# Kernel tuning notes

Hardware: AMD Instinct MI355X
Metric: run time of the kernel (lower is better)

Reference implementation:

```python
import jax, jax.numpy as jnp
from jax import lax
import numpy as np

B, L, N = 128, 16, 20000
H_IN, H, H_T = 512, 1024, 128


def setup_inputs() -> dict:
    key = jax.random.key(0)
    ks = jax.random.split(key, 8)
    def xav(k, shape):
        fan_in, fan_out = shape[1], shape[0]
        a = jnp.sqrt(6.0 / (fan_in + fan_out))
        return jax.random.uniform(k, shape, jnp.float32, -a, a)
    v = jax.random.uniform(ks[0], (B, L, N), jnp.float32)
    t = jax.random.uniform(ks[1], (B, L), jnp.float32)
    W_down = xav(ks[2], (H_IN, N))
    Wt_up_w = xav(ks[3], (H_T, 1))
    Wt_up_b = jnp.zeros((H_T,), jnp.float32)
    W_vt = xav(ks[4], (H_IN, H_IN + H_T))
    k_lstm = 1.0 / jnp.sqrt(H)
    W_ih = jax.random.uniform(ks[5], (4 * H, H_IN), jnp.float32, -k_lstm, k_lstm)
    W_hh = jax.random.uniform(ks[6], (4 * H, H), jnp.float32, -k_lstm, k_lstm)
    b_ih = jnp.zeros((4 * H,), jnp.float32)
    b_hh = jnp.zeros((4 * H,), jnp.float32)
    lin_w = xav(ks[7], (1, H))
    lin_b = jnp.zeros((1,), jnp.float32)
    return {"v": v, "t": t, "W_down": W_down, "Wt_up_w": Wt_up_w,
            "Wt_up_b": Wt_up_b, "W_vt": W_vt, "W_ih": W_ih, "W_hh": W_hh,
            "b_ih": b_ih, "b_hh": b_hh, "lin_w": lin_w, "lin_b": lin_b}


def reference(v, t, W_down, Wt_up_w, Wt_up_b, W_vt, W_ih, W_hh, b_ih, b_hh, lin_w, lin_b):
    b, rw_len, n = v.shape
    h_dim = W_hh.shape[1]
    # W_down: [B,L,N] @ [N,H_in] -> [B,L,H_in]
    vd = jnp.einsum('bln,dn->bld', v, W_down)
    # Wt_up: scalar time -> [B,L,H_t]
    te = t[..., None] * Wt_up_w[:, 0] + Wt_up_b
    vt = jnp.concatenate([vd, te], axis=-1)          # [B,L,H_in+H_t]
    inputs = jnp.einsum('blk,ik->bli', vt, W_vt)     # [B,L,H_in]
    # precompute input-side LSTM gate projections for all steps
    xg = jnp.einsum('bli,gi->blg', inputs, W_ih) + b_ih  # [B,L,4H]
    xg = jnp.swapaxes(xg, 0, 1)                      # [L,B,4H] for scan

    def step(carry, xg_t):
        h, c = carry
        gates = xg_t + h @ W_hh.T + b_hh             # [B,4H]
        i, f, g, o = jnp.split(gates, 4, axis=-1)    # PyTorch gate order i,f,g,o
        i = jax.nn.sigmoid(i)
        f = jax.nn.sigmoid(f)
        g = jnp.tanh(g)
        o = jax.nn.sigmoid(o)
        c = f * c + i * g
        h = o * jnp.tanh(c)
        return (h, c), None

    h0 = jnp.zeros((b, h_dim), v.dtype)
    c0 = jnp.zeros((b, h_dim), v.dtype)
    (h, _), _ = lax.scan(step, (h0, c0), xg)
    pred = h @ lin_w.T + lin_b                       # [B,1]
    return pred
```

## Files before the change

### kernel.cpp

```cpp
#include <hip/hip_runtime.h>

typedef _Float16 f16;
typedef _Float16 f16x2 __attribute__((ext_vector_type(2)));
typedef _Float16 f16x4 __attribute__((ext_vector_type(4)));
typedef _Float16 f16x8 __attribute__((ext_vector_type(8)));
typedef float f32x4 __attribute__((ext_vector_type(4)));

__device__ __forceinline__ f32x4 mfma16(f16x8 a, f16x8 b, f32x4 c) {
  return __builtin_amdgcn_mfma_f32_16x16x32_f16(a, b, c, 0, 0, 0);
}

__device__ __forceinline__ float sigmoid_(float x) { return 1.f / (1.f + __expf(-x)); }
__device__ __forceinline__ float tanh_(float x) { return 1.f - 2.f / (__expf(2.f * x) + 1.f); }

__global__ void cvt_kernel(const float* __restrict__ src, f16* __restrict__ dst, int n4) {
  int i = blockIdx.x * 256 + threadIdx.x;
  if (i < n4) {
    float4 v = ((const float4*)src)[i];
    f16x4 h = {(f16)v.x, (f16)v.y, (f16)v.z, (f16)v.w};
    ((f16x4*)dst)[i] = h;
  }
}

__global__ __launch_bounds__(256, 2) void gemm1_kernel(
    const float* __restrict__ A, const f16* __restrict__ B, f16* __restrict__ P) {
  constexpr int K = 20000;
  __shared__ f16 Al[128][40];
  __shared__ f16 Bl[128][40];
  int tid = threadIdx.x;
  int split = blockIdx.x;
  int m0 = (blockIdx.y >> 2) * 128, n0 = (blockIdx.y & 3) * 128;
  int it0 = (split * 625) >> 3, it1 = ((split + 1) * 625) >> 3;
  int wid = tid >> 6, lane = tid & 63;
  int wm = wid & 1, wn = wid >> 1;
  int lm = lane & 15, quad = lane >> 4;
  int srow = tid >> 1, sseg = (tid & 1) * 16;

  const float* aptr = A + (size_t)(m0 + srow) * K + sseg;
  const f16* bptr = B + (size_t)(n0 + srow) * K + sseg;

  float4 Ar0, Ar1, Ar2, Ar3;
  f16x8 Br0, Br1;
  {
    int k0 = it0 * 32;
    Ar0 = *(const float4*)(aptr + k0);
    Ar1 = *(const float4*)(aptr + k0 + 4);
    Ar2 = *(const float4*)(aptr + k0 + 8);
    Ar3 = *(const float4*)(aptr + k0 + 12);
    Br0 = *(const f16x8*)(bptr + k0);
    Br1 = *(const f16x8*)(bptr + k0 + 8);
  }

  f32x4 acc[4][4];
#pragma unroll
  for (int i = 0; i < 4; ++i)
#pragma unroll
    for (int j = 0; j < 4; ++j) acc[i][j] = (f32x4){0.f, 0.f, 0.f, 0.f};

  for (int it = it0; it < it1; ++it) {
    __syncthreads();
    f16x8 pa0 = {(f16)Ar0.x, (f16)Ar0.y, (f16)Ar0.z, (f16)Ar0.w,
                 (f16)Ar1.x, (f16)Ar1.y, (f16)Ar1.z, (f16)Ar1.w};
    f16x8 pa1 = {(f16)Ar2.x, (f16)Ar2.y, (f16)Ar2.z, (f16)Ar2.w,
                 (f16)Ar3.x, (f16)Ar3.y, (f16)Ar3.z, (f16)Ar3.w};
    *(f16x8*)&Al[srow][sseg] = pa0;
    *(f16x8*)&Al[srow][sseg + 8] = pa1;
    *(f16x8*)&Bl[srow][sseg] = Br0;
    *(f16x8*)&Bl[srow][sseg + 8] = Br1;
    if (it + 1 < it1) {
      int kn = (it + 1) * 32;
      Ar0 = *(const float4*)(aptr + kn);
      Ar1 = *(const float4*)(aptr + kn + 4);
      Ar2 = *(const float4*)(aptr + kn + 8);
      Ar3 = *(const float4*)(aptr + kn + 12);
      Br0 = *(const f16x8*)(bptr + kn);
      Br1 = *(const f16x8*)(bptr + kn + 8);
    }
    __syncthreads();
    f16x8 af[4], bf[4];
#pragma unroll
    for (int mi = 0; mi < 4; ++mi) af[mi] = *(const f16x8*)&Al[wm * 64 + mi * 16 + lm][quad * 8];
#pragma unroll
    for (int ni = 0; ni < 4; ++ni) bf[ni] = *(const f16x8*)&Bl[wn * 64 + ni * 16 + lm][quad * 8];
#pragma unroll
    for (int mi = 0; mi < 4; ++mi)
#pragma unroll
      for (int ni = 0; ni < 4; ++ni) acc[mi][ni] = mfma16(af[mi], bf[ni], acc[mi][ni]);
  }
  size_t base = (size_t)split * 2048;
#pragma unroll
  for (int mi = 0; mi < 4; ++mi)
#pragma unroll
    for (int ni = 0; ni < 4; ++ni)
#pragma unroll
      for (int r = 0; r < 4; ++r) {
        int row = m0 + wm * 64 + mi * 16 + quad * 4 + r;
        int col = n0 + wn * 64 + ni * 16 + lm;
        P[(base + row) * 512 + col] = (f16)acc[mi][ni][r];
      }
}

__global__ void build_vt_kernel(const f16* __restrict__ P, const float* __restrict__ t,
                                const float* __restrict__ wtw, const float* __restrict__ wtb,
                                f16* __restrict__ vt) {
  int m = blockIdx.x;
  float tv = t[m];
  for (int c = threadIdx.x; c < 640; c += 256) {
    float val;
    if (c < 512) {
      val = 0.f;
#pragma unroll
      for (int s = 0; s < 8; ++s) val += (float)P[((size_t)s * 2048 + m) * 512 + c];
    } else {
      val = tv * wtw[c - 512] + wtb[c - 512];
    }
    vt[(size_t)m * 640 + c] = (f16)val;
  }
}

template <int EPI>
__global__ __launch_bounds__(256, 2) void gemm128_kernel(
    const f16* __restrict__ A, const f16* __restrict__ B, f16* __restrict__ out,
    const float* __restrict__ bias0, const float* __restrict__ bias1, int K_iters, int N) {
  __shared__ f16 Al[128][40];
  __shared__ f16 Bl[128][40];
  int tid = threadIdx.x;
  int m0 = blockIdx.y * 128, n0 = blockIdx.x * 128;
  int wid = tid >> 6, lane = tid & 63;
  int wm = wid & 1, wn = wid >> 1;
  int lm = lane & 15, quad = lane >> 4;
  int K = K_iters * 32;

  f32x4 acc[4][4];
#pragma unroll
  for (int i = 0; i < 4; ++i)
#pragma unroll
    for (int j = 0; j < 4; ++j) acc[i][j] = (f32x4){0.f, 0.f, 0.f, 0.f};

  for (int it = 0; it < K_iters; ++it) {
    int k0 = it * 32;
    __syncthreads();
#pragma unroll
    for (int i = 0; i < 2; ++i) {
      int slot = tid + i * 256;
      int row = slot >> 2, seg = slot & 3;
      *(f16x8*)&Al[row][seg * 8] = *(const f16x8*)(A + (size_t)(m0 + row) * K + k0 + seg * 8);
      *(f16x8*)&Bl[row][seg * 8] = *(const f16x8*)(B + (size_t)(n0 + row) * K + k0 + seg * 8);
    }
    __syncthreads();
    f16x8 af[4], bf[4];
#pragma unroll
    for (int mi = 0; mi < 4; ++mi) af[mi] = *(const f16x8*)&Al[wm * 64 + mi * 16 + lm][quad * 8];
#pragma unroll
    for (int ni = 0; ni < 4; ++ni) bf[ni] = *(const f16x8*)&Bl[wn * 64 + ni * 16 + lm][quad * 8];
#pragma unroll
    for (int mi = 0; mi < 4; ++mi)
#pragma unroll
      for (int ni = 0; ni < 4; ++ni) acc[mi][ni] = mfma16(af[mi], bf[ni], acc[mi][ni]);
  }
#pragma unroll
  for (int mi = 0; mi < 4; ++mi)
#pragma unroll
    for (int ni = 0; ni < 4; ++ni)
#pragma unroll
      for (int r = 0; r < 4; ++r) {
        int row = m0 + wm * 64 + mi * 16 + quad * 4 + r;
        int col = n0 + wn * 64 + ni * 16 + lm;
        float val = acc[mi][ni][r];
        if (EPI == 0) {
          out[(size_t)row * N + col] = (f16)val;
        } else {
          int l = row & 15, b = row >> 4;
          out[(size_t)(l * 128 + b) * N + col] = (f16)(val + bias0[col] + bias1[col]);
        }
      }
}

__global__ __launch_bounds__(256, 1) void lstm_step2_kernel(
    const f16* __restrict__ h_in, const f16* __restrict__ Whh,
    const f16* __restrict__ xg_l, float* __restrict__ cT, f16* __restrict__ h_out) {
  __shared__ f16 Alf[32 * 1032];
  __shared__ float gl[4][32][17];
  __shared__ f16 hx[32][18];
  int tid = threadIdx.x;
  int w = tid >> 6, lane = tid & 63;
  int lm = lane & 15, quad = lane >> 4;
  int h0 = blockIdx.x * 16;
  int b0 = blockIdx.y * 32;

#pragma unroll
  for (int i = 0; i < 16; ++i) {
    int idx = i * 256 + tid;
    int r = idx >> 7, c8 = (idx & 127) * 8;
    *(f16x8*)&Alf[r * 1032 + c8] = *(const f16x8*)(h_in + (size_t)(b0 + r) * 1024 + c8);
  }
  const f16* wrow = Whh + ((size_t)(w << 10) + h0 + lm) * 1024 + quad * 8;
  f16x8 Bv[8];
#pragma unroll
  for (int j = 0; j < 8; ++j) Bv[j] = *(const f16x8*)(wrow + j * 32);
  f32x4 acc0 = {0.f, 0.f, 0.f, 0.f}, acc1 = {0.f, 0.f, 0.f, 0.f};
  __syncthreads();
#pragma unroll
  for (int it = 0; it < 32; ++it) {
    f16x8 bfr = Bv[it & 7];
    if (it < 24) Bv[it & 7] = *(const f16x8*)(wrow + (it + 8) * 32);
    f16x8 a0 = *(const f16x8*)&Alf[lm * 1032 + it * 32 + quad * 8];
    f16x8 a1 = *(const f16x8*)&Alf[(16 + lm) * 1032 + it * 32 + quad * 8];
    acc0 = mfma16(a0, bfr, acc0);
    acc1 = mfma16(a1, bfr, acc1);
  }
#pragma unroll
  for (int r = 0; r < 4; ++r) {
    gl[w][quad * 4 + r][lm] = acc0[r];
    gl[w][16 + quad * 4 + r][lm] = acc1[r];
  }
  __syncthreads();
#pragma unroll
  for (int half = 0; half < 2; ++half) {
    int b = tid & 31, hl = (tid >> 5) + half * 8;
    int gb = b0 + b, gh = h0 + hl;
    const f16* xr = xg_l + (size_t)gb * 4096 + gh;
    float gi = (float)xr[0] + gl[0][b][hl];
    float gf = (float)xr[1024] + gl[1][b][hl];
    float gg = (float)xr[2048] + gl[2][b][hl];
    float go = (float)xr[3072] + gl[3][b][hl];
    float iv = sigmoid_(gi), fv = sigmoid_(gf), gv = tanh_(gg), ov = sigmoid_(go);
    size_t ci = (size_t)gh * 128 + gb;
    float cc = fv * cT[ci] + iv * gv;
    cT[ci] = cc;
    hx[b][hl] = (f16)(ov * tanh_(cc));
  }
  __syncthreads();
  {
    int b = tid >> 3, e = (tid & 7) * 2;
    f16x2 hv = {hx[b][e], hx[b][e + 1]};
    *(f16x2*)(h_out + (size_t)(b0 + b) * 1024 + h0 + e) = hv;
  }
}

__global__ void pred_kernel(const f16* __restrict__ h, const float* __restrict__ w,
                            const float* __restrict__ b, float* __restrict__ out) {
  int bb = blockIdx.x, tid = threadIdx.x;
  f16x4 hv = *(const f16x4*)(h + (size_t)bb * 1024 + tid * 4);
  float4 wv = *(const float4*)(w + tid * 4);
  float s = (float)hv[0] * wv.x + (float)hv[1] * wv.y + (float)hv[2] * wv.z + (float)hv[3] * wv.w;
#pragma unroll
  for (int off = 32; off > 0; off >>= 1) s += __shfl_down(s, off);
  __shared__ float red[4];
  if ((tid & 63) == 0) red[tid >> 6] = s;
  __syncthreads();
  if (tid == 0) out[bb] = red[0] + red[1] + red[2] + red[3] + b[0];
}

extern "C" void kernel_launch(void* const* d_in, const int* in_sizes, int n_in,
                              void* d_out, int out_size, void* d_ws, size_t ws_size,
                              hipStream_t stream) {
  (void)in_sizes; (void)n_in; (void)out_size; (void)ws_size;
  const float* v      = (const float*)d_in[0];
  const float* t      = (const float*)d_in[1];
  const float* W_down = (const float*)d_in[2];
  const float* Wt_w   = (const float*)d_in[3];
  const float* Wt_b   = (const float*)d_in[4];
  const float* W_vt   = (const float*)d_in[5];
  const float* W_ih   = (const float*)d_in[6];
  const float* W_hh   = (const float*)d_in[7];
  const float* b_ih   = (const float*)d_in[8];
  const float* b_hh   = (const float*)d_in[9];
  const float* lin_w  = (const float*)d_in[10];
  const float* lin_b  = (const float*)d_in[11];

  char* ws = (char*)d_ws;
  constexpr size_t OFF_WDOWN = 0;
  constexpr size_t OFF_WVT   = 20480000;
  constexpr size_t OFF_WIH   = 21135360;
  constexpr size_t OFF_WHH   = 25329664;
  constexpr size_t OFF_VT    = 33718272;
  constexpr size_t OFF_IN    = 36339712;
  constexpr size_t OFF_XG    = 38436864;
  constexpr size_t OFF_H0    = 55214080;
  constexpr size_t OFF_C     = 55476224;
  constexpr size_t OFF_H1    = 56000512;

  f16* wdown16 = (f16*)(ws + OFF_WDOWN);
  f16* wvt16   = (f16*)(ws + OFF_WVT);
  f16* wih16   = (f16*)(ws + OFF_WIH);
  f16* whh16   = (f16*)(ws + OFF_WHH);
  f16* vt16    = (f16*)(ws + OFF_VT);
  f16* in16    = (f16*)(ws + OFF_IN);
  f16* pxg     = (f16*)(ws + OFF_XG);
  float* cT    = (float*)(ws + OFF_C);
  f16* hb[2]   = {(f16*)(ws + OFF_H0), (f16*)(ws + OFF_H1)};

  hipMemsetAsync(ws + OFF_H0, 0, 786432, stream);

  cvt_kernel<<<10000, 256, 0, stream>>>(W_down, wdown16, 2560000);
  cvt_kernel<<<320, 256, 0, stream>>>(W_vt, wvt16, 81920);
  cvt_kernel<<<2048, 256, 0, stream>>>(W_ih, wih16, 524288);
  cvt_kernel<<<4096, 256, 0, stream>>>(W_hh, whh16, 1048576);

  gemm1_kernel<<<dim3(8, 64), 256, 0, stream>>>(v, wdown16, pxg);
  build_vt_kernel<<<2048, 256, 0, stream>>>(pxg, t, Wt_w, Wt_b, vt16);
  gemm128_kernel<0><<<dim3(4, 16), 256, 0, stream>>>(vt16, wvt16, in16, nullptr, nullptr, 20, 512);
  gemm128_kernel<1><<<dim3(32, 16), 256, 0, stream>>>(in16, wih16, pxg, b_ih, b_hh, 16, 4096);

  for (int s = 0; s < 16; ++s) {
    lstm_step2_kernel<<<dim3(64, 4), 256, 0, stream>>>(
        hb[s & 1], whh16, pxg + (size_t)s * 128 * 4096, cT, hb[(s + 1) & 1]);
  }
  pred_kernel<<<128, 256, 0, stream>>>(hb[0], lin_w, lin_b, (float*)d_out);
}
```

Before: 544.5 us.

## Fuse W_down conversion into GEMM, merge weight casts, retile small GEMMs

The separate fp32->fp16 pass over W_down is dropped. gemm1 now loads fp32 W_down directly and converts it in registers, which removes a full write and re-read of a 20 MB weight. The split-K factor for gemm1 goes from 8 to 16 with higher occupancy, and build_vt sums 16 partials. The remaining three weight casts are merged into one launch, and the two follow-up GEMMs use smaller templated tiles so more blocks run. The tradeoff is twice the partial-sum traffic and more conversion work inside the main GEMM loop.

```diff
diff --git a/kernel.cpp b/kernel.cpp
--- a/kernel.cpp
+++ b/kernel.cpp
@@ -13,42 +13,52 @@
 __device__ __forceinline__ float sigmoid_(float x) { return 1.f / (1.f + __expf(-x)); }
 __device__ __forceinline__ float tanh_(float x) { return 1.f - 2.f / (__expf(2.f * x) + 1.f); }
 
-__global__ void cvt_kernel(const float* __restrict__ src, f16* __restrict__ dst, int n4) {
+__global__ void cvt3_kernel(const float* __restrict__ s0, f16* __restrict__ d0, int n0,
+                            const float* __restrict__ s1, f16* __restrict__ d1, int n1,
+                            const float* __restrict__ s2, f16* __restrict__ d2, int n2) {
   int i = blockIdx.x * 256 + threadIdx.x;
-  if (i < n4) {
-    float4 v = ((const float4*)src)[i];
-    f16x4 h = {(f16)v.x, (f16)v.y, (f16)v.z, (f16)v.w};
-    ((f16x4*)dst)[i] = h;
-  }
-}
-
-__global__ __launch_bounds__(256, 2) void gemm1_kernel(
-    const float* __restrict__ A, const f16* __restrict__ B, f16* __restrict__ P) {
+  const float* s;
+  f16* d;
+  int j;
+  if (i < n0) {
+    s = s0; d = d0; j = i;
+  } else if (i < n0 + n1) {
+    s = s1; d = d1; j = i - n0;
+  } else if (i < n0 + n1 + n2) {
+    s = s2; d = d2; j = i - n0 - n1;
+  } else {
+    return;
+  }
+  float4 v = ((const float4*)s)[j];
+  f16x4 h = {(f16)v.x, (f16)v.y, (f16)v.z, (f16)v.w};
+  ((f16x4*)d)[j] = h;
+}
+
+__global__ __launch_bounds__(256, 3) void gemm1_kernel(
+    const float* __restrict__ A, const float* __restrict__ B, f16* __restrict__ P) {
   constexpr int K = 20000;
-  __shared__ f16 Al[128][40];
-  __shared__ f16 Bl[128][40];
+  __shared__ f16 Al[128][44];
+  __shared__ f16 Bl[128][44];
   int tid = threadIdx.x;
   int split = blockIdx.x;
   int m0 = (blockIdx.y >> 2) * 128, n0 = (blockIdx.y & 3) * 128;
-  int it0 = (split * 625) >> 3, it1 = ((split + 1) * 625) >> 3;
+  int it0 = (split * 625) >> 4, it1 = ((split + 1) * 625) >> 4;
   int wid = tid >> 6, lane = tid & 63;
   int wm = wid & 1, wn = wid >> 1;
   int lm = lane & 15, quad = lane >> 4;
   int srow = tid >> 1, sseg = (tid & 1) * 16;
 
   const float* aptr = A + (size_t)(m0 + srow) * K + sseg;
-  const f16* bptr = B + (size_t)(n0 + srow) * K + sseg;
-
-  float4 Ar0, Ar1, Ar2, Ar3;
-  f16x8 Br0, Br1;
+  const float* bptr = B + (size_t)(n0 + srow) * K + sseg;
+
+  float4 Ar[4], Br[4];
   {
     int k0 = it0 * 32;
-    Ar0 = *(const float4*)(aptr + k0);
-    Ar1 = *(const float4*)(aptr + k0 + 4);
-    Ar2 = *(const float4*)(aptr + k0 + 8);
-    Ar3 = *(const float4*)(aptr + k0 + 12);
-    Br0 = *(const f16x8*)(bptr + k0);
-    Br1 = *(const f16x8*)(bptr + k0 + 8);
+#pragma unroll
+    for (int j = 0; j < 4; ++j) {
+      Ar[j] = *(const float4*)(aptr + k0 + j * 4);
+      Br[j] = *(const float4*)(bptr + k0 + j * 4);
+    }
   }
 
   f32x4 acc[4][4];
@@ -59,33 +69,38 @@
 
   for (int it = it0; it < it1; ++it) {
     __syncthreads();
-    f16x8 pa0 = {(f16)Ar0.x, (f16)Ar0.y, (f16)Ar0.z, (f16)Ar0.w,
-                 (f16)Ar1.x, (f16)Ar1.y, (f16)Ar1.z, (f16)Ar1.w};
-    f16x8 pa1 = {(f16)Ar2.x, (f16)Ar2.y, (f16)Ar2.z, (f16)Ar2.w,
-                 (f16)Ar3.x, (f16)Ar3.y, (f16)Ar3.z, (f16)Ar3.w};
-    *(f16x8*)&Al[srow][sseg] = pa0;
-    *(f16x8*)&Al[srow][sseg + 8] = pa1;
-    *(f16x8*)&Bl[srow][sseg] = Br0;
-    *(f16x8*)&Bl[srow][sseg + 8] = Br1;
+    {
+      f16x8 pa0 = {(f16)Ar[0].x, (f16)Ar[0].y, (f16)Ar[0].z, (f16)Ar[0].w,
+                   (f16)Ar[1].x, (f16)Ar[1].y, (f16)Ar[1].z, (f16)Ar[1].w};
+      f16x8 pa1 = {(f16)Ar[2].x, (f16)Ar[2].y, (f16)Ar[2].z, (f16)Ar[2].w,
+                   (f16)Ar[3].x, (f16)Ar[3].y, (f16)Ar[3].z, (f16)Ar[3].w};
+      f16x8 pb0 = {(f16)Br[0].x, (f16)Br[0].y, (f16)Br[0].z, (f16)Br[0].w,
+                   (f16)Br[1].x, (f16)Br[1].y, (f16)Br[1].z, (f16)Br[1].w};
+      f16x8 pb1 = {(f16)Br[2].x, (f16)Br[2].y, (f16)Br[2].z, (f16)Br[2].w,
+                   (f16)Br[3].x, (f16)Br[3].y, (f16)Br[3].z, (f16)Br[3].w};
+      *(f16x8*)&Al[srow][sseg] = pa0;
+      *(f16x8*)&Al[srow][sseg + 8] = pa1;
+      *(f16x8*)&Bl[srow][sseg] = pb0;
+      *(f16x8*)&Bl[srow][sseg + 8] = pb1;
+    }
     if (it + 1 < it1) {
       int kn = (it + 1) * 32;
-      Ar0 = *(const float4*)(aptr + kn);
-      Ar1 = *(const float4*)(aptr + kn + 4);
-      Ar2 = *(const float4*)(aptr + kn + 8);
-      Ar3 = *(const float4*)(aptr + kn + 12);
-      Br0 = *(const f16x8*)(bptr + kn);
-      Br1 = *(const f16x8*)(bptr + kn + 8);
+#pragma unroll
+      for (int j = 0; j < 4; ++j) {
+        Ar[j] = *(const float4*)(aptr + kn + j * 4);
+        Br[j] = *(const float4*)(bptr + kn + j * 4);
+      }
     }
     __syncthreads();
-    f16x8 af[4], bf[4];
+    f16x8 af[4];
 #pragma unroll
     for (int mi = 0; mi < 4; ++mi) af[mi] = *(const f16x8*)&Al[wm * 64 + mi * 16 + lm][quad * 8];
 #pragma unroll
-    for (int ni = 0; ni < 4; ++ni) bf[ni] = *(const f16x8*)&Bl[wn * 64 + ni * 16 + lm][quad * 8];
-#pragma unroll
-    for (int mi = 0; mi < 4; ++mi)
-#pragma unroll
-      for (int ni = 0; ni < 4; ++ni) acc[mi][ni] = mfma16(af[mi], bf[ni], acc[mi][ni]);
+    for (int ni = 0; ni < 4; ++ni) {
+      f16x8 bf = *(const f16x8*)&Bl[wn * 64 + ni * 16 + lm][quad * 8];
+#pragma unroll
+      for (int mi = 0; mi < 4; ++mi) acc[mi][ni] = mfma16(af[mi], bf, acc[mi][ni]);
+    }
   }
   size_t base = (size_t)split * 2048;
 #pragma unroll
@@ -110,7 +125,7 @@
     if (c < 512) {
       val = 0.f;
 #pragma unroll
-      for (int s = 0; s < 8; ++s) val += (float)P[((size_t)s * 2048 + m) * 512 + c];
+      for (int s = 0; s < 16; ++s) val += (float)P[((size_t)s * 2048 + m) * 512 + c];
     } else {
       val = tv * wtw[c - 512] + wtb[c - 512];
     }
@@ -118,54 +133,61 @@
   }
 }
 
-template <int EPI>
-__global__ __launch_bounds__(256, 2) void gemm128_kernel(
+template <int TM, int TN, int EPI>
+__global__ __launch_bounds__(256, 4) void gemmT_kernel(
     const f16* __restrict__ A, const f16* __restrict__ B, f16* __restrict__ out,
-    const float* __restrict__ bias0, const float* __restrict__ bias1, int K_iters, int N) {
-  __shared__ f16 Al[128][40];
-  __shared__ f16 Bl[128][40];
+    const float* __restrict__ bias0, const float* __restrict__ bias1, int K_iters, int K,
+    int N) {
+  constexpr int FM = TM / 32, FN = TN / 32;
+  __shared__ f16 Al[TM][40];
+  __shared__ f16 Bl[TN][40];
   int tid = threadIdx.x;
-  int m0 = blockIdx.y * 128, n0 = blockIdx.x * 128;
+  int m0 = blockIdx.y * TM, n0 = blockIdx.x * TN;
   int wid = tid >> 6, lane = tid & 63;
   int wm = wid & 1, wn = wid >> 1;
   int lm = lane & 15, quad = lane >> 4;
-  int K = K_iters * 32;
-
-  f32x4 acc[4][4];
-#pragma unroll
-  for (int i = 0; i < 4; ++i)
-#pragma unroll
-    for (int j = 0; j < 4; ++j) acc[i][j] = (f32x4){0.f, 0.f, 0.f, 0.f};
+
+  f32x4 acc[FM][FN];
+#pragma unroll
+  for (int i = 0; i < FM; ++i)
+#pragma unroll
+    for (int j = 0; j < FN; ++j) acc[i][j] = (f32x4){0.f, 0.f, 0.f, 0.f};
 
   for (int it = 0; it < K_iters; ++it) {
     int k0 = it * 32;
     __syncthreads();
 #pragma unroll
-    for (int i = 0; i < 2; ++i) {
-      int slot = tid + i * 256;
+    for (int r = 0; r < TM / 64; ++r) {
+      int slot = r * 256 + tid;
       int row = slot >> 2, seg = slot & 3;
       *(f16x8*)&Al[row][seg * 8] = *(const f16x8*)(A + (size_t)(m0 + row) * K + k0 + seg * 8);
+    }
+#pragma unroll
+    for (int r = 0; r < TN / 64; ++r) {
+      int slot = r * 256 + tid;
+      int row = slot >> 2, seg = slot & 3;
       *(f16x8*)&Bl[row][seg * 8] = *(const f16x8*)(B + (size_t)(n0 + row) * K + k0 + seg * 8);
     }
     __syncthreads();
-    f16x8 af[4], bf[4];
-#pragma unroll
-    for (int mi = 0; mi < 4; ++mi) af[mi] = *(const f16x8*)&Al[wm * 64 + mi * 16 + lm][quad * 8];
-#pragma unroll
-    for (int ni = 0; ni < 4; ++ni) bf[ni] = *(const f16x8*)&Bl[wn * 64 + ni * 16 + lm][quad * 8];
-#pragma unroll
-    for (int mi = 0; mi < 4; ++mi)
-#pragma unroll
-      for (int ni = 0; ni < 4; ++ni) acc[mi][ni] = mfma16(af[mi], bf[ni], acc[mi][ni]);
-  }
-#pragma unroll
-  for (int mi = 0; mi < 4; ++mi)
-#pragma unroll
-    for (int ni = 0; ni < 4; ++ni)
+    f16x8 af[FM];
+#pragma unroll
+    for (int mi = 0; mi < FM; ++mi)
+      af[mi] = *(const f16x8*)&Al[wm * (TM / 2) + mi * 16 + lm][quad * 8];
+#pragma unroll
+    for (int ni = 0; ni < FN; ++ni) {
+      f16x8 bf = *(const f16x8*)&Bl[wn * (TN / 2) + ni * 16 + lm][quad * 8];
+#pragma unroll
+      for (int mi = 0; mi < FM; ++mi) acc[mi][ni] = mfma16(af[mi], bf, acc[mi][ni]);
+    }
+  }
+#pragma unroll
+  for (int mi = 0; mi < FM; ++mi)
+#pragma unroll
+    for (int ni = 0; ni < FN; ++ni)
 #pragma unroll
       for (int r = 0; r < 4; ++r) {
-        int row = m0 + wm * 64 + mi * 16 + quad * 4 + r;
-        int col = n0 + wn * 64 + ni * 16 + lm;
+        int row = m0 + wm * (TM / 2) + mi * 16 + quad * 4 + r;
+        int col = n0 + wn * (TN / 2) + ni * 16 + lm;
         float val = acc[mi][ni][r];
         if (EPI == 0) {
           out[(size_t)row * N + col] = (f16)val;
@@ -270,38 +292,36 @@
   const float* lin_b  = (const float*)d_in[11];
 
   char* ws = (char*)d_ws;
-  constexpr size_t OFF_WDOWN = 0;
-  constexpr size_t OFF_WVT   = 20480000;
-  constexpr size_t OFF_WIH   = 21135360;
-  constexpr size_t OFF_WHH   = 25329664;
-  constexpr size_t OFF_VT    = 33718272;
-  constexpr size_t OFF_IN    = 36339712;
-  constexpr size_t OFF_XG    = 38436864;
-  constexpr size_t OFF_H0    = 55214080;
-  constexpr size_t OFF_C     = 55476224;
-  constexpr size_t OFF_H1    = 56000512;
-
-  f16* wdown16 = (f16*)(ws + OFF_WDOWN);
-  f16* wvt16   = (f16*)(ws + OFF_WVT);
-  f16* wih16   = (f16*)(ws + OFF_WIH);
-  f16* whh16   = (f16*)(ws + OFF_WHH);
-  f16* vt16    = (f16*)(ws + OFF_VT);
-  f16* in16    = (f16*)(ws + OFF_IN);
-  f16* pxg     = (f16*)(ws + OFF_XG);
-  float* cT    = (float*)(ws + OFF_C);
-  f16* hb[2]   = {(f16*)(ws + OFF_H0), (f16*)(ws + OFF_H1)};
+  constexpr size_t OFF_WVT = 0;
+  constexpr size_t OFF_WIH = 655360;
+  constexpr size_t OFF_WHH = 4849664;
+  constexpr size_t OFF_VT  = 13238272;
+  constexpr size_t OFF_IN  = 15859712;
+  constexpr size_t OFF_P   = 17956864;
+  constexpr size_t OFF_H0  = 51511296;
+  constexpr size_t OFF_C   = 51773440;
+  constexpr size_t OFF_H1  = 52297728;
+
+  f16* wvt16  = (f16*)(ws + OFF_WVT);
+  f16* wih16  = (f16*)(ws + OFF_WIH);
+  f16* whh16  = (f16*)(ws + OFF_WHH);
+  f16* vt16   = (f16*)(ws + OFF_VT);
+  f16* in16   = (f16*)(ws + OFF_IN);
+  f16* pxg    = (f16*)(ws + OFF_P);
+  float* cT   = (float*)(ws + OFF_C);
+  f16* hb[2]  = {(f16*)(ws + OFF_H0), (f16*)(ws + OFF_H1)};
 
   hipMemsetAsync(ws + OFF_H0, 0, 786432, stream);
 
-  cvt_kernel<<<10000, 256, 0, stream>>>(W_down, wdown16, 2560000);
-  cvt_kernel<<<320, 256, 0, stream>>>(W_vt, wvt16, 81920);
-  cvt_kernel<<<2048, 256, 0, stream>>>(W_ih, wih16, 524288);
-  cvt_kernel<<<4096, 256, 0, stream>>>(W_hh, whh16, 1048576);
-
-  gemm1_kernel<<<dim3(8, 64), 256, 0, stream>>>(v, wdown16, pxg);
+  cvt3_kernel<<<6465, 256, 0, stream>>>(W_vt, wvt16, 81920, W_ih, wih16, 524288, W_hh, whh16,
+                                        1048576);
+
+  gemm1_kernel<<<dim3(16, 64), 256, 0, stream>>>(v, W_down, pxg);
   build_vt_kernel<<<2048, 256, 0, stream>>>(pxg, t, Wt_w, Wt_b, vt16);
-  gemm128_kernel<0><<<dim3(4, 16), 256, 0, stream>>>(vt16, wvt16, in16, nullptr, nullptr, 20, 512);
-  gemm128_kernel<1><<<dim3(32, 16), 256, 0, stream>>>(in16, wih16, pxg, b_ih, b_hh, 16, 4096);
+  gemmT_kernel<64, 64, 0><<<dim3(8, 32), 256, 0, stream>>>(vt16, wvt16, in16, nullptr, nullptr,
+                                                           20, 640, 512);
+  gemmT_kernel<64, 128, 1><<<dim3(32, 32), 256, 0, stream>>>(in16, wih16, pxg, b_ih, b_hh, 16,
+                                                             512, 4096);
 
   for (int s = 0; s < 16; ++s) {
     lstm_step2_kernel<<<dim3(64, 4), 256, 0, stream>>>(
```

Measured after the change: 554.8 us. Within noise of the previous version (+1.9%).
